# Kernel optimization log

Measured on AMD Instinct MI355X. Metric: run time of the kernel, lower is better.

## Reference

```python
import jax, jax.numpy as jnp
import numpy as np

N, T, n, C, C2 = 4, 8, 16384, 64, 64

def setup_inputs() -> dict:
    key = jax.random.key(0)
    k1, k2, k3, k4, k5 = jax.random.split(key, 5)
    return {
        "key_mem": jax.random.normal(k1, (N, T, n, C), dtype=jnp.float32),
        "val_mem": jax.random.normal(k2, (N, T, n, C2), dtype=jnp.float32),
        "key_cur": jax.random.normal(k3, (N, n, C), dtype=jnp.float32),
        "val_cur": jax.random.normal(k4, (N, n, C2), dtype=jnp.float32),
        "alpha": jax.random.normal(k5, (1,), dtype=jnp.float32),
    }

def reference(key_mem, val_mem, key_cur, val_cur, alpha):
    # kv_mul: contract memory tokens (T*n) -> (N, C, C2), tiny matrix
    kv_mul = jnp.einsum('btnc,btnd->bcd', key_mem, val_mem)
    # softmax over the C axis (dim=1 in torch layout (N, C, C2))
    kv_mul = jax.nn.softmax(kv_mul, axis=1)
    # out: (N, n, C) @ (N, C, C2) -> (N, n, C2)
    out = jnp.einsum('bnc,bcd->bnd', key_cur, kv_mul)
    return alpha * out + val_cur
```

## Files before the change

kernel.cpp:

```cpp
#include <hip/hip_runtime.h>
#include <math.h>

#define N_TOK   16384
#define K_TOT   (8 * N_TOK)
#define N_BATCH 4
#define BPB     128
#define RPB     (K_TOT / BPB)
#define BK      64
#define NBUF    (RPB / BK)

typedef const __attribute__((address_space(1))) unsigned int* as1_u32p;
typedef __attribute__((address_space(3))) unsigned int* as3_u32p;

__device__ __forceinline__ void gload16(const float* g, float* l) {
  __builtin_amdgcn_global_load_lds((as1_u32p)g, (as3_u32p)l, 16, 0, 0);
}

__global__ __launch_bounds__(512, 4) void k1_accum(
    const float* __restrict__ key, const float* __restrict__ val,
    float* __restrict__ part) {
  __shared__ float lds[16384];
  int blk  = blockIdx.x;
  int b    = blk / BPB;
  int p    = blk % BPB;
  int wave = threadIdx.x >> 6;
  int lane = threadIdx.x & 63;
  int i = lane >> 3;
  int j = lane & 7;

  size_t row0 = (size_t)b * K_TOT + (size_t)p * RPB;
  const float* kb = key + row0 * 64;
  const float* vb = val + row0 * 64;

  float acc[8][8];
#pragma unroll
  for (int a = 0; a < 8; a++)
#pragma unroll
    for (int c = 0; c < 8; c++) acc[a][c] = 0.f;

  auto stage = [&](int t, int buf) {
    const float* kg = kb + (size_t)t * (BK * 64);
    const float* vg = vb + (size_t)t * (BK * 64);
    float* dl = &lds[buf * 8192];
    gload16(kg + wave * 256 + lane * 4,        dl + wave * 256);
    gload16(kg + (wave + 8) * 256 + lane * 4,  dl + (wave + 8) * 256);
    gload16(vg + wave * 256 + lane * 4,        dl + 4096 + wave * 256);
    gload16(vg + (wave + 8) * 256 + lane * 4,  dl + 4096 + (wave + 8) * 256);
  };

  stage(0, 0);
  for (int t = 0; t < NBUF; t++) {
    __syncthreads();
    if (t + 1 < NBUF) stage(t + 1, (t + 1) & 1);
    const float* ks = &lds[(t & 1) * 8192];
    const float* vs = ks + 4096;
#pragma unroll
    for (int rr = 0; rr < BK / 8; rr++) {
      int r = wave + rr * 8;
      float4 k0 = *(const float4*)&ks[r * 64 + 8 * i];
      float4 k1 = *(const float4*)&ks[r * 64 + 8 * i + 4];
      float4 v0 = *(const float4*)&vs[r * 64 + 8 * j];
      float4 v1 = *(const float4*)&vs[r * 64 + 8 * j + 4];
      float kr[8] = {k0.x, k0.y, k0.z, k0.w, k1.x, k1.y, k1.z, k1.w};
      float vr[8] = {v0.x, v0.y, v0.z, v0.w, v1.x, v1.y, v1.z, v1.w};
#pragma unroll
      for (int a = 0; a < 8; a++)
#pragma unroll
        for (int c = 0; c < 8; c++)
          acc[a][c] = fmaf(kr[a], vr[c], acc[a][c]);
    }
  }

  float (*red)[4096] = (float(*)[4096])lds;
  if (wave < 2) {
#pragma unroll
    for (int a = 0; a < 8; a++) {
      int c = 8 * i + a;
      *(float4*)&red[wave][c * 64 + 8 * j] =
          make_float4(acc[a][0], acc[a][1], acc[a][2], acc[a][3]);
      *(float4*)&red[wave][c * 64 + 8 * j + 4] =
          make_float4(acc[a][4], acc[a][5], acc[a][6], acc[a][7]);
    }
  }
  __syncthreads();
#pragma unroll
  for (int g = 1; g < 4; g++) {
    if (wave >= 2 * g && wave < 2 * g + 2) {
      int wb = wave - 2 * g;
#pragma unroll
      for (int a = 0; a < 8; a++) {
        int c = 8 * i + a;
        float4* d0 = (float4*)&red[wb][c * 64 + 8 * j];
        float4* d1 = (float4*)&red[wb][c * 64 + 8 * j + 4];
        float4 x0 = *d0, x1 = *d1;
        *d0 = make_float4(x0.x + acc[a][0], x0.y + acc[a][1],
                          x0.z + acc[a][2], x0.w + acc[a][3]);
        *d1 = make_float4(x1.x + acc[a][4], x1.y + acc[a][5],
                          x1.z + acc[a][6], x1.w + acc[a][7]);
      }
    }
    __syncthreads();
  }

  float* dst = part + (size_t)blk * 4096;
  int t = threadIdx.x;
#pragma unroll
  for (int x = 0; x < 8; x++) {
    int e = t + 512 * x;
    dst[e] = red[0][e] + red[1][e];
  }
}

__global__ __launch_bounds__(256, 4) void k2_reduce(
    const float* __restrict__ part, float* __restrict__ kv, int bpb) {
  int b  = blockIdx.x >> 6;
  int c  = blockIdx.x & 63;
  int p4 = threadIdx.x >> 6;
  int d  = threadIdx.x & 63;

  float s = 0.f;
  int iters = bpb >> 2;
  const float* src = part + (size_t)(b * bpb) * 4096 + c * 64 + d;
#pragma unroll 4
  for (int x = 0; x < iters; x++) s += src[(size_t)(p4 + 4 * x) * 4096];

  __shared__ float l[256];
  l[threadIdx.x] = s;
  __syncthreads();
  if (p4 == 0)
    kv[((size_t)b * 64 + c) * 64 + d] = l[d] + l[64 + d] + l[128 + d] + l[192 + d];
}

__global__ __launch_bounds__(64, 1) void k2b_softmax(
    const float* __restrict__ kv, float* __restrict__ P) {
  int b = blockIdx.x;
  int d = threadIdx.x;
  const float* s = kv + (size_t)b * 4096 + d;
  float v[64];
#pragma unroll
  for (int c = 0; c < 64; c++) v[c] = s[c * 64];
  float mx = v[0];
#pragma unroll
  for (int c = 1; c < 64; c++) mx = fmaxf(mx, v[c]);
  float sum = 0.f;
#pragma unroll
  for (int c = 0; c < 64; c++) {
    v[c] = __expf(v[c] - mx);
    sum += v[c];
  }
  float inv = 1.f / sum;
  float* o = P + (size_t)b * 4096 + d;
#pragma unroll
  for (int c = 0; c < 64; c++) o[c * 64] = v[c] * inv;
}

__global__ __launch_bounds__(256, 4) void k3_out(
    const float* __restrict__ P, const float* __restrict__ keyc,
    const float* __restrict__ valc, const float* __restrict__ alphap,
    float* __restrict__ out) {
  __shared__ float Ps[4096];
  __shared__ float kT[64 * 68];

  int bb = blockIdx.x >> 8;
  int mb = blockIdx.x & 255;
  int m0 = mb * 64;
  int t = threadIdx.x;

  const float4* p4 = (const float4*)(P + (size_t)bb * 4096);
  float4* ps4 = (float4*)Ps;
#pragma unroll
  for (int u = 0; u < 4; u++) ps4[t + 256 * u] = p4[t + 256 * u];

  int r  = t >> 2;
  int cb = (t & 3) * 16;
  const float* krow = keyc + ((size_t)bb * N_TOK + m0 + r) * 64;
#pragma unroll
  for (int u = 0; u < 4; u++) {
    float4 kk = *(const float4*)&krow[cb + 4 * u];
    int c = cb + 4 * u;
    kT[(c + 0) * 68 + r] = kk.x;
    kT[(c + 1) * 68 + r] = kk.y;
    kT[(c + 2) * 68 + r] = kk.z;
    kT[(c + 3) * 68 + r] = kk.w;
  }
  __syncthreads();

  int wave = t >> 6, lane = t & 63;
  int mi = lane >> 3, j = lane & 7;
  int m = wave * 16 + mi * 2;

  float acc[2][8];
#pragma unroll
  for (int a = 0; a < 2; a++)
#pragma unroll
    for (int d = 0; d < 8; d++) acc[a][d] = 0.f;

#pragma unroll 4
  for (int c = 0; c < 64; c++) {
    float2 kk = *(const float2*)&kT[c * 68 + m];
    float4 p0 = *(const float4*)&Ps[c * 64 + 8 * j];
    float4 p1 = *(const float4*)&Ps[c * 64 + 8 * j + 4];
    float pr[8] = {p0.x, p0.y, p0.z, p0.w, p1.x, p1.y, p1.z, p1.w};
#pragma unroll
    for (int d = 0; d < 8; d++) {
      acc[0][d] = fmaf(kk.x, pr[d], acc[0][d]);
      acc[1][d] = fmaf(kk.y, pr[d], acc[1][d]);
    }
  }

  float alpha = alphap[0];
#pragma unroll
  for (int a = 0; a < 2; a++) {
    size_t off = ((size_t)bb * N_TOK + m0 + m + a) * 64 + 8 * j;
    float4 v0 = *(const float4*)&valc[off];
    float4 v1 = *(const float4*)&valc[off + 4];
    float4 o0 = make_float4(fmaf(alpha, acc[a][0], v0.x),
                            fmaf(alpha, acc[a][1], v0.y),
                            fmaf(alpha, acc[a][2], v0.z),
                            fmaf(alpha, acc[a][3], v0.w));
    float4 o1 = make_float4(fmaf(alpha, acc[a][4], v1.x),
                            fmaf(alpha, acc[a][5], v1.y),
                            fmaf(alpha, acc[a][6], v1.z),
                            fmaf(alpha, acc[a][7], v1.w));
    *(float4*)&out[off] = o0;
    *(float4*)&out[off + 4] = o1;
  }
}

extern "C" void kernel_launch(void* const* d_in, const int* in_sizes, int n_in,
                              void* d_out, int out_size, void* d_ws,
                              size_t ws_size, hipStream_t stream) {
  const float* key_mem = (const float*)d_in[0];
  const float* val_mem = (const float*)d_in[1];
  const float* key_cur = (const float*)d_in[2];
  const float* val_cur = (const float*)d_in[3];
  const float* alpha   = (const float*)d_in[4];
  float* out = (float*)d_out;
  float* ws  = (float*)d_ws;

  float* part = ws;
  float* kv   = ws + (size_t)(N_BATCH * BPB) * 4096;
  float* P    = ws;

  k1_accum<<<N_BATCH * BPB, 512, 0, stream>>>(key_mem, val_mem, part);
  k2_reduce<<<256, 256, 0, stream>>>(part, kv, BPB);
  k2b_softmax<<<N_BATCH, 64, 0, stream>>>(kv, P);
  k3_out<<<N_BATCH * (N_TOK / 64), 256, 0, stream>>>(P, key_cur, val_cur,
                                                     alpha, out);
}
```

Baseline: 343.1 us.

## Give each wave a private contiguous row range with double-buffered LDS staging

Instead of the whole block staging 64-row tiles and synchronizing with __syncthreads each iteration, each wave now owns a contiguous slice of rows and double-buffers 8-row chunks into its own LDS region. It waits on vmcnt with s_waitcnt instead of block barriers. This removes per-tile block-wide barriers and lets waves run independently. The cost is shallower prefetch (8 rows per stage), more loop iterations, and correctness that depends on the hand-coded waitcnt encodings and the compiler not reordering LDS reads.

```diff
diff --git a/kernel.cpp b/kernel.cpp
--- a/kernel.cpp
+++ b/kernel.cpp
@@ -6,8 +6,9 @@
 #define N_BATCH 4
 #define BPB     128
 #define RPB     (K_TOT / BPB)
-#define BK      64
-#define NBUF    (RPB / BK)
+#define RPW     (RPB / 8)
+#define BR      8
+#define NB      (RPW / BR)
 
 typedef const __attribute__((address_space(1))) unsigned int* as1_u32p;
 typedef __attribute__((address_space(3))) unsigned int* as3_u32p;
@@ -15,6 +16,9 @@
 __device__ __forceinline__ void gload16(const float* g, float* l) {
   __builtin_amdgcn_global_load_lds((as1_u32p)g, (as3_u32p)l, 16, 0, 0);
 }
+
+#define WAITCNT_VM4  0x0F74
+#define WAITCNT_VM0  0x0F70
 
 __global__ __launch_bounds__(512, 4) void k1_accum(
     const float* __restrict__ key, const float* __restrict__ val,
@@ -28,9 +32,10 @@
   int i = lane >> 3;
   int j = lane & 7;
 
-  size_t row0 = (size_t)b * K_TOT + (size_t)p * RPB;
+  size_t row0 = (size_t)b * K_TOT + (size_t)p * RPB + (size_t)wave * RPW;
   const float* kb = key + row0 * 64;
   const float* vb = val + row0 * 64;
+  float* wl = &lds[wave * 2048];
 
   float acc[8][8];
 #pragma unroll
@@ -38,29 +43,38 @@
 #pragma unroll
     for (int c = 0; c < 8; c++) acc[a][c] = 0.f;
 
-  auto stage = [&](int t, int buf) {
-    const float* kg = kb + (size_t)t * (BK * 64);
-    const float* vg = vb + (size_t)t * (BK * 64);
-    float* dl = &lds[buf * 8192];
-    gload16(kg + wave * 256 + lane * 4,        dl + wave * 256);
-    gload16(kg + (wave + 8) * 256 + lane * 4,  dl + (wave + 8) * 256);
-    gload16(vg + wave * 256 + lane * 4,        dl + 4096 + wave * 256);
-    gload16(vg + (wave + 8) * 256 + lane * 4,  dl + 4096 + (wave + 8) * 256);
-  };
-
-  stage(0, 0);
-  for (int t = 0; t < NBUF; t++) {
-    __syncthreads();
-    if (t + 1 < NBUF) stage(t + 1, (t + 1) & 1);
-    const float* ks = &lds[(t & 1) * 8192];
-    const float* vs = ks + 4096;
-#pragma unroll
-    for (int rr = 0; rr < BK / 8; rr++) {
-      int r = wave + rr * 8;
-      float4 k0 = *(const float4*)&ks[r * 64 + 8 * i];
-      float4 k1 = *(const float4*)&ks[r * 64 + 8 * i + 4];
-      float4 v0 = *(const float4*)&vs[r * 64 + 8 * j];
-      float4 v1 = *(const float4*)&vs[r * 64 + 8 * j + 4];
+  {
+    const float* kg = kb;
+    const float* vg = vb;
+    gload16(kg + lane * 4,       wl);
+    gload16(kg + 256 + lane * 4, wl + 256);
+    gload16(vg + lane * 4,       wl + 512);
+    gload16(vg + 256 + lane * 4, wl + 768);
+  }
+
+  for (int t = 0; t < NB; t++) {
+    if (t + 1 < NB) {
+      const float* kg = kb + (size_t)(t + 1) * (BR * 64);
+      const float* vg = vb + (size_t)(t + 1) * (BR * 64);
+      float* d = wl + ((t + 1) & 1) * 1024;
+      gload16(kg + lane * 4,       d);
+      gload16(kg + 256 + lane * 4, d + 256);
+      gload16(vg + lane * 4,       d + 512);
+      gload16(vg + 256 + lane * 4, d + 768);
+      __builtin_amdgcn_s_waitcnt(WAITCNT_VM4);
+    } else {
+      __builtin_amdgcn_s_waitcnt(WAITCNT_VM0);
+    }
+    asm volatile("" ::: "memory");
+
+    const float* ks = wl + (t & 1) * 1024;
+    const float* vs = ks + 512;
+#pragma unroll
+    for (int rr = 0; rr < BR; rr++) {
+      float4 k0 = *(const float4*)&ks[rr * 64 + 8 * i];
+      float4 k1 = *(const float4*)&ks[rr * 64 + 8 * i + 4];
+      float4 v0 = *(const float4*)&vs[rr * 64 + 8 * j];
+      float4 v1 = *(const float4*)&vs[rr * 64 + 8 * j + 4];
       float kr[8] = {k0.x, k0.y, k0.z, k0.w, k1.x, k1.y, k1.z, k1.w};
       float vr[8] = {v0.x, v0.y, v0.z, v0.w, v1.x, v1.y, v1.z, v1.w};
 #pragma unroll
@@ -69,8 +83,10 @@
         for (int c = 0; c < 8; c++)
           acc[a][c] = fmaf(kr[a], vr[c], acc[a][c]);
     }
-  }
-
+    asm volatile("" ::: "memory");
+  }
+
+  __syncthreads();
   float (*red)[4096] = (float(*)[4096])lds;
   if (wave < 2) {
 #pragma unroll
```

Result: no change. 345.4 us (+0.6%).

## Compute key-value contraction with split-bf16 MFMA and parallelize softmax across waves

Applied to the files above, without the earlier changes.

Replaces the scalar FMA outer-product accumulation in the first kernel with bf16 MFMA instructions. Each fp32 input is split into high and low bf16 parts, and three MFMA products are accumulated to approximate fp32 accuracy. Inputs are loaded into registers and written transposed into LDS while the next chunk is prefetched. This removes the cross-wave LDS reduction, since each wave owns an output tile. The softmax kernel now runs one wave per (batch, column) using shuffle reductions instead of four single-wave blocks, at the cost of a small precision loss from dropping the low×low term.

```diff
diff --git a/kernel.cpp b/kernel.cpp
--- a/kernel.cpp
+++ b/kernel.cpp
@@ -6,108 +6,115 @@
 #define N_BATCH 4
 #define BPB     128
 #define RPB     (K_TOT / BPB)
-#define BK      64
-#define NBUF    (RPB / BK)
-
-typedef const __attribute__((address_space(1))) unsigned int* as1_u32p;
-typedef __attribute__((address_space(3))) unsigned int* as3_u32p;
-
-__device__ __forceinline__ void gload16(const float* g, float* l) {
-  __builtin_amdgcn_global_load_lds((as1_u32p)g, (as3_u32p)l, 16, 0, 0);
-}
-
-__global__ __launch_bounds__(512, 4) void k1_accum(
+#define CHUNK   64
+#define NCH     (RPB / CHUNK)
+#define PITCH_U 36
+#define PART_U  (64 * PITCH_U)
+
+typedef short short8 __attribute__((ext_vector_type(8)));
+typedef float f32x4  __attribute__((ext_vector_type(4)));
+
+union FragU { uint4 u; short8 s; };
+
+__device__ __forceinline__ uint bf16_rne(float f, float* rounded) {
+  uint u = __float_as_uint(f);
+  uint r = u + 0x7FFFu + ((u >> 16) & 1u);
+  *rounded = __uint_as_float(r & 0xFFFF0000u);
+  return r >> 16;
+}
+
+__global__ __launch_bounds__(512, 2) void k1_mfma(
     const float* __restrict__ key, const float* __restrict__ val,
     float* __restrict__ part) {
-  __shared__ float lds[16384];
+  __shared__ uint lds[4 * PART_U];
+
   int blk  = blockIdx.x;
   int b    = blk / BPB;
   int p    = blk % BPB;
-  int wave = threadIdx.x >> 6;
-  int lane = threadIdx.x & 63;
-  int i = lane >> 3;
-  int j = lane & 7;
-
-  size_t row0 = (size_t)b * K_TOT + (size_t)p * RPB;
-  const float* kb = key + row0 * 64;
-  const float* vb = val + row0 * 64;
-
-  float acc[8][8];
-#pragma unroll
-  for (int a = 0; a < 8; a++)
-#pragma unroll
-    for (int c = 0; c < 8; c++) acc[a][c] = 0.f;
-
-  auto stage = [&](int t, int buf) {
-    const float* kg = kb + (size_t)t * (BK * 64);
-    const float* vg = vb + (size_t)t * (BK * 64);
-    float* dl = &lds[buf * 8192];
-    gload16(kg + wave * 256 + lane * 4,        dl + wave * 256);
-    gload16(kg + (wave + 8) * 256 + lane * 4,  dl + (wave + 8) * 256);
-    gload16(vg + wave * 256 + lane * 4,        dl + 4096 + wave * 256);
-    gload16(vg + (wave + 8) * 256 + lane * 4,  dl + 4096 + (wave + 8) * 256);
+  int t    = threadIdx.x;
+  int wave = t >> 6;
+  int lane = t & 63;
+
+  int arr = t >> 8;
+  int tt  = t & 255;
+  int c0  = (tt & 15) * 4;
+  int r0  = (tt >> 4) * 4;
+  const float* src = arr ? val : key;
+  size_t rowbase = (size_t)b * K_TOT + (size_t)p * RPB;
+  uint sbase = arr * 2 * PART_U;
+
+  int mt  = wave >> 1;
+  int ntb = (wave & 1) * 2;
+  int m16 = lane & 15;
+  int ko  = lane >> 4;
+
+  f32x4 acc[2] = {{0.f, 0.f, 0.f, 0.f}, {0.f, 0.f, 0.f, 0.f}};
+  float4 ld[4];
+
+  auto load_chunk = [&](int ch) {
+#pragma unroll
+    for (int q = 0; q < 4; q++)
+      ld[q] = *(const float4*)&src[(rowbase + (size_t)ch * CHUNK + r0 + q) * 64 + c0];
   };
 
-  stage(0, 0);
-  for (int t = 0; t < NBUF; t++) {
+  auto write_chunk = [&]() {
+#pragma unroll
+    for (int cc = 0; cc < 4; cc++) {
+      uint h[4], l[4];
+#pragma unroll
+      for (int q = 0; q < 4; q++) {
+        float f = (&ld[q].x)[cc];
+        float hf;
+        h[q] = bf16_rne(f, &hf);
+        float dummy;
+        l[q] = bf16_rne(f - hf, &dummy);
+      }
+      uint2 hp = make_uint2(h[0] | (h[1] << 16), h[2] | (h[3] << 16));
+      uint2 lp = make_uint2(l[0] | (l[1] << 16), l[2] | (l[3] << 16));
+      uint base = sbase + (uint)(c0 + cc) * PITCH_U + (uint)(r0 >> 1);
+      *(uint2*)&lds[base]          = hp;
+      *(uint2*)&lds[base + PART_U] = lp;
+    }
+  };
+
+  load_chunk(0);
+  write_chunk();
+  __syncthreads();
+
+  for (int ch = 0; ch < NCH; ch++) {
+    if (ch + 1 < NCH) load_chunk(ch + 1);
+
+#pragma unroll
+    for (int ks = 0; ks < 2; ks++) {
+      uint ao = (uint)(mt * 16 + m16) * PITCH_U + ks * 16 + ko * 4;
+      FragU Ah, Al;
+      Ah.u = *(const uint4*)&lds[ao];
+      Al.u = *(const uint4*)&lds[ao + PART_U];
+#pragma unroll
+      for (int nn = 0; nn < 2; nn++) {
+        uint bo = 2 * PART_U + (uint)((ntb + nn) * 16 + m16) * PITCH_U + ks * 16 + ko * 4;
+        FragU Bh, Bl;
+        Bh.u = *(const uint4*)&lds[bo];
+        Bl.u = *(const uint4*)&lds[bo + PART_U];
+        acc[nn] = __builtin_amdgcn_mfma_f32_16x16x32_bf16(Ah.s, Bh.s, acc[nn], 0, 0, 0);
+        acc[nn] = __builtin_amdgcn_mfma_f32_16x16x32_bf16(Ah.s, Bl.s, acc[nn], 0, 0, 0);
+        acc[nn] = __builtin_amdgcn_mfma_f32_16x16x32_bf16(Al.s, Bh.s, acc[nn], 0, 0, 0);
+      }
+    }
     __syncthreads();
-    if (t + 1 < NBUF) stage(t + 1, (t + 1) & 1);
-    const float* ks = &lds[(t & 1) * 8192];
-    const float* vs = ks + 4096;
-#pragma unroll
-    for (int rr = 0; rr < BK / 8; rr++) {
-      int r = wave + rr * 8;
-      float4 k0 = *(const float4*)&ks[r * 64 + 8 * i];
-      float4 k1 = *(const float4*)&ks[r * 64 + 8 * i + 4];
-      float4 v0 = *(const float4*)&vs[r * 64 + 8 * j];
-      float4 v1 = *(const float4*)&vs[r * 64 + 8 * j + 4];
-      float kr[8] = {k0.x, k0.y, k0.z, k0.w, k1.x, k1.y, k1.z, k1.w};
-      float vr[8] = {v0.x, v0.y, v0.z, v0.w, v1.x, v1.y, v1.z, v1.w};
-#pragma unroll
-      for (int a = 0; a < 8; a++)
-#pragma unroll
-        for (int c = 0; c < 8; c++)
-          acc[a][c] = fmaf(kr[a], vr[c], acc[a][c]);
-    }
-  }
-
-  float (*red)[4096] = (float(*)[4096])lds;
-  if (wave < 2) {
-#pragma unroll
-    for (int a = 0; a < 8; a++) {
-      int c = 8 * i + a;
-      *(float4*)&red[wave][c * 64 + 8 * j] =
-          make_float4(acc[a][0], acc[a][1], acc[a][2], acc[a][3]);
-      *(float4*)&red[wave][c * 64 + 8 * j + 4] =
-          make_float4(acc[a][4], acc[a][5], acc[a][6], acc[a][7]);
-    }
-  }
-  __syncthreads();
-#pragma unroll
-  for (int g = 1; g < 4; g++) {
-    if (wave >= 2 * g && wave < 2 * g + 2) {
-      int wb = wave - 2 * g;
-#pragma unroll
-      for (int a = 0; a < 8; a++) {
-        int c = 8 * i + a;
-        float4* d0 = (float4*)&red[wb][c * 64 + 8 * j];
-        float4* d1 = (float4*)&red[wb][c * 64 + 8 * j + 4];
-        float4 x0 = *d0, x1 = *d1;
-        *d0 = make_float4(x0.x + acc[a][0], x0.y + acc[a][1],
-                          x0.z + acc[a][2], x0.w + acc[a][3]);
-        *d1 = make_float4(x1.x + acc[a][4], x1.y + acc[a][5],
-                          x1.z + acc[a][6], x1.w + acc[a][7]);
-      }
-    }
+    if (ch + 1 < NCH) write_chunk();
     __syncthreads();
   }
 
   float* dst = part + (size_t)blk * 4096;
-  int t = threadIdx.x;
-#pragma unroll
-  for (int x = 0; x < 8; x++) {
-    int e = t + 512 * x;
-    dst[e] = red[0][e] + red[1][e];
+#pragma unroll
+  for (int nn = 0; nn < 2; nn++) {
+    int d = (ntb + nn) * 16 + m16;
+#pragma unroll
+    for (int r = 0; r < 4; r++) {
+      int c = mt * 16 + ko * 4 + r;
+      dst[c * 64 + d] = acc[nn][r];
+    }
   }
 }
 
@@ -131,27 +138,20 @@
     kv[((size_t)b * 64 + c) * 64 + d] = l[d] + l[64 + d] + l[128 + d] + l[192 + d];
 }
 
-__global__ __launch_bounds__(64, 1) void k2b_softmax(
+__global__ __launch_bounds__(64, 4) void k2b_softmax(
     const float* __restrict__ kv, float* __restrict__ P) {
-  int b = blockIdx.x;
-  int d = threadIdx.x;
-  const float* s = kv + (size_t)b * 4096 + d;
-  float v[64];
-#pragma unroll
-  for (int c = 0; c < 64; c++) v[c] = s[c * 64];
-  float mx = v[0];
-#pragma unroll
-  for (int c = 1; c < 64; c++) mx = fmaxf(mx, v[c]);
-  float sum = 0.f;
-#pragma unroll
-  for (int c = 0; c < 64; c++) {
-    v[c] = __expf(v[c] - mx);
-    sum += v[c];
-  }
-  float inv = 1.f / sum;
-  float* o = P + (size_t)b * 4096 + d;
-#pragma unroll
-  for (int c = 0; c < 64; c++) o[c * 64] = v[c] * inv;
+  int b = blockIdx.x >> 6;
+  int d = blockIdx.x & 63;
+  int c = threadIdx.x;
+  float v = kv[(size_t)b * 4096 + c * 64 + d];
+  float mx = v;
+#pragma unroll
+  for (int o = 32; o; o >>= 1) mx = fmaxf(mx, __shfl_xor(mx, o, 64));
+  float e = __expf(v - mx);
+  float s = e;
+#pragma unroll
+  for (int o = 32; o; o >>= 1) s += __shfl_xor(s, o, 64);
+  P[(size_t)b * 4096 + c * 64 + d] = e / s;
 }
 
 __global__ __launch_bounds__(256, 4) void k3_out(
@@ -242,9 +242,9 @@
   float* kv   = ws + (size_t)(N_BATCH * BPB) * 4096;
   float* P    = ws;
 
-  k1_accum<<<N_BATCH * BPB, 512, 0, stream>>>(key_mem, val_mem, part);
+  k1_mfma<<<N_BATCH * BPB, 512, 0, stream>>>(key_mem, val_mem, part);
   k2_reduce<<<256, 256, 0, stream>>>(part, kv, BPB);
-  k2b_softmax<<<N_BATCH, 64, 0, stream>>>(kv, P);
+  k2b_softmax<<<N_BATCH * 64, 64, 0, stream>>>(kv, P);
   k3_out<<<N_BATCH * (N_TOK / 64), 256, 0, stream>>>(P, key_cur, val_cur,
                                                      alpha, out);
 }
```

After: 322.3 us. 6.1% less time.
